# Optimization experiments

Measured on AMD Instinct MI355X. Metric: run time of the kernel, lower is better.

The kernel has to match this reference:

```python
import jax, jax.numpy as jnp
import numpy as np

EPS = 1e-7  # tf.keras.backend.epsilon()
DEGREE = 5
SCALE_BASE = 1.0
SCALE_LEGENDRE = 1.0


def legendre_basis(x, degree):
    # min/max normalization over the feature axis -> x_norm in [-1, 1]
    x_min = jnp.min(x, axis=-1, keepdims=True)
    x_max = jnp.max(x, axis=-1, keepdims=True)
    x_norm = 2.0 * (x - x_min) / (x_max - x_min + EPS) - 1.0
    polys = [jnp.ones_like(x_norm), x_norm]
    for n in range(2, degree + 1):
        p_n = ((2 * n - 1) * x_norm * polys[-1] - (n - 1) * polys[-2]) / n
        polys.append(p_n)
    return jnp.stack(polys, axis=-1)  # [b, i, degree+1]


def setup_inputs() -> dict:
    key = jax.random.key(0)
    k1, k2, k3 = jax.random.split(key, 3)
    b, i, o, d = 4096, 1024, 1024, DEGREE + 1
    x = jax.random.normal(k1, (b, i), dtype=jnp.float32)
    # HeUniform: limit = sqrt(6 / fan_in)
    lim_b = np.sqrt(6.0 / i)
    base_weight = jax.random.uniform(k2, (i, o), dtype=jnp.float32, minval=-lim_b, maxval=lim_b)
    legendre_weight = jax.random.uniform(k3, (i, o, d), dtype=jnp.float32, minval=-lim_b, maxval=lim_b)
    return {"x": x, "base_weight": base_weight, "legendre_weight": legendre_weight}


def reference(x, base_weight, legendre_weight):
    base_output = jax.nn.silu(x @ base_weight)  # [b, o]
    basis = legendre_basis(x, DEGREE)  # [b, i, d]
    # 'bi,iod,bid->bo' == fold x into the basis then contract (i, d)
    xb = x[..., None] * basis  # [b, i, d]
    legendre_output = jnp.einsum('bid,iod->bo', xb, legendre_weight)
    return SCALE_BASE * base_output + SCALE_LEGENDRE * legendre_output
```

## Files before the change

### kernel.cpp

```cpp
#include <hip/hip_runtime.h>
#include <stdint.h>

typedef unsigned short u16;
typedef unsigned int   u32;
typedef __attribute__((ext_vector_type(8))) short bhalf8;
typedef __attribute__((ext_vector_type(4))) float f32x4;

#define B_ROWS 4096
#define I_DIM  1024
#define O_DIM  1024
#define N_D    6
#define K_LEG  (I_DIM * N_D)

#define BM 256
#define BN 256
#define BK 32
#define NU 56
#define SLOT_BYTES 32768
#define LDS_BYTES  131072

__device__ __forceinline__ u16 f2b(float f) {
  u32 u = __float_as_uint(f);
  return (u16)((u + 0x7fffu + ((u >> 16) & 1u)) >> 16);
}

__device__ __forceinline__ void gld_lds16(const void* g, void* l) {
  __builtin_amdgcn_global_load_lds(
      (const __attribute__((address_space(1))) u32*)(uintptr_t)g,
      (__attribute__((address_space(3))) u32*)(u32)(uintptr_t)l, 16, 0, 0);
}

__global__ void k_prep_bbT(const float* __restrict__ bw, u16* __restrict__ Bb) {
  __shared__ float t[32][33];
  const int bx = blockIdx.x & 31, by = blockIdx.x >> 5;
  const int i0 = by * 32, o0 = bx * 32;
  const int c = threadIdx.x & 31, r0 = threadIdx.x >> 5;
  #pragma unroll
  for (int k = 0; k < 4; ++k) {
    int r = r0 + k * 8;
    t[r][c] = bw[(size_t)(i0 + r) * O_DIM + o0 + c];
  }
  __syncthreads();
  #pragma unroll
  for (int k = 0; k < 4; ++k) {
    int r = r0 + k * 8;
    Bb[(size_t)(o0 + r) * I_DIM + i0 + c] = f2b(t[c][r]);
  }
}

#define RS 201
__global__ void k_prep_blT(const float* __restrict__ lw, u16* __restrict__ Bl) {
  __shared__ float t[32 * RS];
  const int bx = blockIdx.x & 31, by = blockIdx.x >> 5;
  const int i0 = by * 32, o0 = bx * 32;
  for (int q = threadIdx.x; q < 32 * 48; q += 256) {
    int ri = q / 48, s4 = q % 48;
    float4 v = *(const float4*)(lw + (size_t)(i0 + ri) * (O_DIM * N_D) + o0 * N_D + s4 * 4);
    float* p = t + ri * RS + s4 * 4;
    p[0] = v.x; p[1] = v.y; p[2] = v.z; p[3] = v.w;
  }
  __syncthreads();
  for (int q = threadIdx.x; q < 32 * 96; q += 256) {
    int ro = q / 96, k = q % 96;
    int e0 = 2 * k, e1 = 2 * k + 1;
    float v0 = t[(e0 / 6) * RS + ro * 6 + (e0 % 6)];
    float v1 = t[(e1 / 6) * RS + ro * 6 + (e1 % 6)];
    u32* dst = (u32*)(Bl + (size_t)(o0 + ro) * K_LEG + i0 * N_D);
    dst[k] = (u32)f2b(v0) | ((u32)f2b(v1) << 16);
  }
}

__global__ void k_prep_basis(const float* __restrict__ x,
                             u16* __restrict__ Ab, u16* __restrict__ Al) {
  int b = blockIdx.x;
  int t = threadIdx.x;
  float4 v = ((const float4*)(x + (size_t)b * I_DIM))[t];
  float mn = fminf(fminf(v.x, v.y), fminf(v.z, v.w));
  float mx = fmaxf(fmaxf(v.x, v.y), fmaxf(v.z, v.w));
  #pragma unroll
  for (int off = 32; off > 0; off >>= 1) {
    mn = fminf(mn, __shfl_xor(mn, off, 64));
    mx = fmaxf(mx, __shfl_xor(mx, off, 64));
  }
  __shared__ float smn[4], smx[4];
  if ((t & 63) == 0) { smn[t >> 6] = mn; smx[t >> 6] = mx; }
  __syncthreads();
  mn = fminf(fminf(smn[0], smn[1]), fminf(smn[2], smn[3]));
  mx = fmaxf(fmaxf(smx[0], smx[1]), fmaxf(smx[2], smx[3]));
  float sc = 2.0f / (mx - mn + 1e-7f);

  float xs[4] = {v.x, v.y, v.z, v.w};
  u32 lb[12];
  #pragma unroll
  for (int e = 0; e < 4; ++e) {
    float xv = xs[e];
    float xn = (xv - mn) * sc - 1.0f;
    float p0 = 1.0f, p1 = xn;
    float p2 = (3.0f * xn * p1 - 1.0f * p0) * (1.0f / 2.0f);
    float p3 = (5.0f * xn * p2 - 2.0f * p1) * (1.0f / 3.0f);
    float p4 = (7.0f * xn * p3 - 3.0f * p2) * (1.0f / 4.0f);
    float p5 = (9.0f * xn * p4 - 4.0f * p3) * (1.0f / 5.0f);
    lb[e * 3 + 0] = (u32)f2b(xv * p0) | ((u32)f2b(xv * p1) << 16);
    lb[e * 3 + 1] = (u32)f2b(xv * p2) | ((u32)f2b(xv * p3) << 16);
    lb[e * 3 + 2] = (u32)f2b(xv * p4) | ((u32)f2b(xv * p5) << 16);
  }
  u32 a0 = (u32)f2b(xs[0]) | ((u32)f2b(xs[1]) << 16);
  u32 a1 = (u32)f2b(xs[2]) | ((u32)f2b(xs[3]) << 16);
  *(uint2*)(Ab + (size_t)b * I_DIM + t * 4) = make_uint2(a0, a1);
  uint4* dl = (uint4*)(Al + (size_t)b * K_LEG + t * 24);
  dl[0] = make_uint4(lb[0], lb[1], lb[2], lb[3]);
  dl[1] = make_uint4(lb[4], lb[5], lb[6], lb[7]);
  dl[2] = make_uint4(lb[8], lb[9], lb[10], lb[11]);
}

__global__ __launch_bounds__(512, 2) void k_gemm(
    const u16* __restrict__ Ab, const u16* __restrict__ Bb,
    const u16* __restrict__ Al, const u16* __restrict__ Bl,
    float* __restrict__ out, float* __restrict__ P) {
  extern __shared__ char lds[];

  const int tid  = threadIdx.x;
  const int wave = tid >> 6;
  const int lane = tid & 63;
  const int wm = wave >> 2;
  const int wn = wave & 3;
  const int rr = lane & 15;
  const int kg = lane >> 4;

  const int bid   = blockIdx.x;
  const int bx    = bid >> 4;
  const int by    = (bid >> 2) & 3;
  const int split = bid & 3;
  const size_t brow = (size_t)bx * BM;
  const size_t bcol = (size_t)by * BN;
  const bool s0 = (split == 0);
  const int legbase = s0 ? 0 : (24 + 56 * (split - 1));

  const int r4 = tid >> 2;
  const size_t cs = (size_t)((((tid & 3) ^ ((r4 >> 1) & 3))) * 8);
  const size_t ar0 = brow + r4,        ar1 = brow + 128 + r4;
  const size_t bc0 = bcol + r4,        bc1 = bcol + 128 + r4;
  char* const l0 = lds + (u32)wave * 1024;

  auto stage = [&](int v) {
    const u16 *sa, *sb; size_t ldk, koff;
    if (s0 && v < 32) { sa = Ab; sb = Bb; ldk = I_DIM; koff = (size_t)v * BK; }
    else {
      size_t lv = s0 ? (size_t)(v - 32) : (size_t)(legbase + v);
      sa = Al; sb = Bl; ldk = K_LEG; koff = lv * BK;
    }
    char* d = l0 + (size_t)(v & 3) * SLOT_BYTES;
    gld_lds16(sa + ar0 * ldk + koff + cs, d);
    gld_lds16(sa + ar1 * ldk + koff + cs, d + 8192);
    gld_lds16(sb + bc0 * ldk + koff + cs, d + 16384);
    gld_lds16(sb + bc1 * ldk + koff + cs, d + 24576);
  };

  const u32 axor  = (u32)((kg ^ ((rr >> 1) & 3)) * 16);
  const u32 abase = (u32)((wm * 128 + rr) * 64) + axor;
  const u32 bbase = 16384u + (u32)((wn * 64 + rr) * 64) + axor;

  f32x4 acc[8][4] = {};

  stage(0); stage(1); stage(2);

#define KITER(u, DO_STAGE, VM)  do {                                          \
    if (DO_STAGE) stage((u) + 3);                                             \
    asm volatile("s_waitcnt vmcnt(" #VM ")" ::: "memory");                    \
    __builtin_amdgcn_s_barrier();                                             \
    asm volatile("" ::: "memory");                                            \
    const char* p_ = lds + (size_t)((u) & 3) * SLOT_BYTES;                    \
    bhalf8 af_[8], bf_[4];                                                    \
    _Pragma("unroll")                                                         \
    for (int n = 0; n < 4; ++n) bf_[n] = *(const bhalf8*)(p_ + bbase + n * 1024); \
    _Pragma("unroll")                                                         \
    for (int m = 0; m < 8; ++m) af_[m] = *(const bhalf8*)(p_ + abase + m * 1024); \
    __builtin_amdgcn_s_setprio(1);                                            \
    _Pragma("unroll")                                                         \
    for (int m = 0; m < 8; ++m)                                               \
      _Pragma("unroll")                                                       \
      for (int n = 0; n < 4; ++n)                                             \
        acc[m][n] = __builtin_amdgcn_mfma_f32_16x16x32_bf16(af_[m], bf_[n], acc[m][n], 0, 0, 0); \
    __builtin_amdgcn_s_setprio(0);                                            \
    asm volatile("s_waitcnt lgkmcnt(0)" ::: "memory");                        \
    __builtin_amdgcn_s_barrier();                                             \
  } while (0)

  for (int u = 0; u < NU - 3; ++u) {
    if (s0 && u == 32) {
      #pragma unroll
      for (int m = 0; m < 8; ++m)
        #pragma unroll
        for (int n = 0; n < 4; ++n)
          #pragma unroll
          for (int j = 0; j < 4; ++j) {
            float v = acc[m][n][j];
            acc[m][n][j] = v / (1.0f + __expf(-v));
          }
    }
    KITER(u, true, 12);
  }
  KITER(53, false, 8);
  KITER(54, false, 4);
  KITER(55, false, 0);
#undef KITER

  float* dst = s0 ? out : (P + (size_t)(split - 1) * ((size_t)B_ROWS * O_DIM));
  #pragma unroll
  for (int m = 0; m < 8; ++m)
    #pragma unroll
    for (int n = 0; n < 4; ++n) {
      const size_t r0 = brow + wm * 128 + m * 16 + kg * 4;
      const size_t c  = bcol + wn * 64 + n * 16 + rr;
      #pragma unroll
      for (int j = 0; j < 4; ++j)
        dst[(r0 + j) * O_DIM + c] = acc[m][n][j];
    }
}

__global__ void k_reduce(float* __restrict__ out, const float* __restrict__ P) {
  const size_t i = (size_t)blockIdx.x * 256 + threadIdx.x;
  const size_t NE = (size_t)B_ROWS * O_DIM / 4;
  float4 a = ((const float4*)out)[i];
  float4 b = ((const float4*)P)[i];
  float4 c = ((const float4*)P)[i + NE];
  float4 d = ((const float4*)P)[i + 2 * NE];
  a.x += b.x + c.x + d.x;  a.y += b.y + c.y + d.y;
  a.z += b.z + c.z + d.z;  a.w += b.w + c.w + d.w;
  ((float4*)out)[i] = a;
}

extern "C" void kernel_launch(void* const* d_in, const int* in_sizes, int n_in,
                              void* d_out, int out_size, void* d_ws, size_t ws_size,
                              hipStream_t stream) {
  const float* x  = (const float*)d_in[0];
  const float* bw = (const float*)d_in[1];
  const float* lw = (const float*)d_in[2];
  float* out = (float*)d_out;

  char* w = (char*)d_ws;
  u16*  Ab = (u16*)(w);
  u16*  Al = (u16*)(w + (size_t)8   * 1024 * 1024);
  u16*  Bb = (u16*)(w + (size_t)56  * 1024 * 1024);
  u16*  Bl = (u16*)(w + (size_t)58  * 1024 * 1024);
  float* P = (float*)(w + (size_t)72 * 1024 * 1024);

  hipFuncSetAttribute((const void*)k_gemm,
                      hipFuncAttributeMaxDynamicSharedMemorySize, LDS_BYTES);

  k_prep_bbT  <<<dim3(1024), 256, 0, stream>>>(bw, Bb);
  k_prep_blT  <<<dim3(1024), 256, 0, stream>>>(lw, Bl);
  k_prep_basis<<<dim3(B_ROWS), 256, 0, stream>>>(x, Ab, Al);
  k_gemm      <<<dim3(4 * (B_ROWS / BM) * (O_DIM / BN)), 512, LDS_BYTES, stream>>>(Ab, Bb, Al, Bl, out, P);
  k_reduce    <<<dim3((B_ROWS * O_DIM / 4) / 256), 256, 0, stream>>>(out, P);
}
```

Measured before the change: 118.0 us.

## Split GEMM k-iteration into two phases with interleaved staging; merge weight prep kernels

Each k-step of the main GEMM becomes two half-phases over the top and bottom four m-tiles. The global-to-LDS loads for A and B are split across the two phases so that LDS reads, async copies and MFMA work interleave more finely. Global pointers are now advanced incrementally instead of recomputed per stage. The two weight transpose/convert kernels are merged into one launch to save a kernel launch. In exchange there are more barriers per k-step, and the vmcnt accounting changes, which risks both ordering bugs and added sync overhead.

```diff
diff --git a/kernel.cpp b/kernel.cpp
--- a/kernel.cpp
+++ b/kernel.cpp
@@ -30,43 +30,44 @@
       (__attribute__((address_space(3))) u32*)(u32)(uintptr_t)l, 16, 0, 0);
 }
 
-__global__ void k_prep_bbT(const float* __restrict__ bw, u16* __restrict__ Bb) {
-  __shared__ float t[32][33];
-  const int bx = blockIdx.x & 31, by = blockIdx.x >> 5;
-  const int i0 = by * 32, o0 = bx * 32;
-  const int c = threadIdx.x & 31, r0 = threadIdx.x >> 5;
-  #pragma unroll
-  for (int k = 0; k < 4; ++k) {
-    int r = r0 + k * 8;
-    t[r][c] = bw[(size_t)(i0 + r) * O_DIM + o0 + c];
-  }
-  __syncthreads();
-  #pragma unroll
-  for (int k = 0; k < 4; ++k) {
-    int r = r0 + k * 8;
-    Bb[(size_t)(o0 + r) * I_DIM + i0 + c] = f2b(t[c][r]);
-  }
-}
-
 #define RS 201
-__global__ void k_prep_blT(const float* __restrict__ lw, u16* __restrict__ Bl) {
+__global__ void k_prep_w(const float* __restrict__ bw, const float* __restrict__ lw,
+                         u16* __restrict__ Bb, u16* __restrict__ Bl) {
   __shared__ float t[32 * RS];
-  const int bx = blockIdx.x & 31, by = blockIdx.x >> 5;
-  const int i0 = by * 32, o0 = bx * 32;
-  for (int q = threadIdx.x; q < 32 * 48; q += 256) {
-    int ri = q / 48, s4 = q % 48;
-    float4 v = *(const float4*)(lw + (size_t)(i0 + ri) * (O_DIM * N_D) + o0 * N_D + s4 * 4);
-    float* p = t + ri * RS + s4 * 4;
-    p[0] = v.x; p[1] = v.y; p[2] = v.z; p[3] = v.w;
-  }
-  __syncthreads();
-  for (int q = threadIdx.x; q < 32 * 96; q += 256) {
-    int ro = q / 96, k = q % 96;
-    int e0 = 2 * k, e1 = 2 * k + 1;
-    float v0 = t[(e0 / 6) * RS + ro * 6 + (e0 % 6)];
-    float v1 = t[(e1 / 6) * RS + ro * 6 + (e1 % 6)];
-    u32* dst = (u32*)(Bl + (size_t)(o0 + ro) * K_LEG + i0 * N_D);
-    dst[k] = (u32)f2b(v0) | ((u32)f2b(v1) << 16);
+  if (blockIdx.x < 1024) {
+    const int bx = blockIdx.x & 31, by = blockIdx.x >> 5;
+    const int i0 = by * 32, o0 = bx * 32;
+    const int c = threadIdx.x & 31, r0 = threadIdx.x >> 5;
+    #pragma unroll
+    for (int k = 0; k < 4; ++k) {
+      int r = r0 + k * 8;
+      t[r * 33 + c] = bw[(size_t)(i0 + r) * O_DIM + o0 + c];
+    }
+    __syncthreads();
+    #pragma unroll
+    for (int k = 0; k < 4; ++k) {
+      int r = r0 + k * 8;
+      Bb[(size_t)(o0 + r) * I_DIM + i0 + c] = f2b(t[c * 33 + r]);
+    }
+  } else {
+    const int blk = blockIdx.x - 1024;
+    const int bx = blk & 31, by = blk >> 5;
+    const int i0 = by * 32, o0 = bx * 32;
+    for (int q = threadIdx.x; q < 32 * 48; q += 256) {
+      int ri = q / 48, s4 = q % 48;
+      float4 v = *(const float4*)(lw + (size_t)(i0 + ri) * (O_DIM * N_D) + o0 * N_D + s4 * 4);
+      float* p = t + ri * RS + s4 * 4;
+      p[0] = v.x; p[1] = v.y; p[2] = v.z; p[3] = v.w;
+    }
+    __syncthreads();
+    for (int q = threadIdx.x; q < 32 * 96; q += 256) {
+      int ro = q / 96, k = q % 96;
+      int e0 = 2 * k, e1 = 2 * k + 1;
+      float v0 = t[(e0 / 6) * RS + ro * 6 + (e0 % 6)];
+      float v1 = t[(e1 / 6) * RS + ro * 6 + (e1 % 6)];
+      u32* dst = (u32*)(Bl + (size_t)(o0 + ro) * K_LEG + i0 * N_D);
+      dst[k] = (u32)f2b(v0) | ((u32)f2b(v1) << 16);
+    }
   }
 }
 
@@ -138,51 +139,79 @@
 
   const int r4 = tid >> 2;
   const size_t cs = (size_t)((((tid & 3) ^ ((r4 >> 1) & 3))) * 8);
-  const size_t ar0 = brow + r4,        ar1 = brow + 128 + r4;
-  const size_t bc0 = bcol + r4,        bc1 = bcol + 128 + r4;
   char* const l0 = lds + (u32)wave * 1024;
 
-  auto stage = [&](int v) {
-    const u16 *sa, *sb; size_t ldk, koff;
-    if (s0 && v < 32) { sa = Ab; sb = Bb; ldk = I_DIM; koff = (size_t)v * BK; }
-    else {
-      size_t lv = s0 ? (size_t)(v - 32) : (size_t)(legbase + v);
-      sa = Al; sb = Bl; ldk = K_LEG; koff = lv * BK;
-    }
-    char* d = l0 + (size_t)(v & 3) * SLOT_BYTES;
-    gld_lds16(sa + ar0 * ldk + koff + cs, d);
-    gld_lds16(sa + ar1 * ldk + koff + cs, d + 8192);
-    gld_lds16(sb + bc0 * ldk + koff + cs, d + 16384);
-    gld_lds16(sb + bc1 * ldk + koff + cs, d + 24576);
+  const u16 *gA0, *gA1, *gB0, *gB1;
+  auto set_ptrs = [&](const u16* A, const u16* Bt, size_t ldk, size_t kt) {
+    const size_t ko = kt * BK + cs;
+    gA0 = A  + (brow + r4) * ldk + ko;
+    gA1 = A  + (brow + 128 + r4) * ldk + ko;
+    gB0 = Bt + (bcol + r4) * ldk + ko;
+    gB1 = Bt + (bcol + 128 + r4) * ldk + ko;
   };
+  if (s0) set_ptrs(Ab, Bb, I_DIM, 0);
+  else    set_ptrs(Al, Bl, K_LEG, (size_t)legbase);
 
   const u32 axor  = (u32)((kg ^ ((rr >> 1) & 3)) * 16);
   const u32 abase = (u32)((wm * 128 + rr) * 64) + axor;
   const u32 bbase = 16384u + (u32)((wn * 64 + rr) * 64) + axor;
 
   f32x4 acc[8][4] = {};
-
-  stage(0); stage(1); stage(2);
-
-#define KITER(u, DO_STAGE, VM)  do {                                          \
-    if (DO_STAGE) stage((u) + 3);                                             \
-    asm volatile("s_waitcnt vmcnt(" #VM ")" ::: "memory");                    \
-    __builtin_amdgcn_s_barrier();                                             \
+  bhalf8 af_[4], af2_[4], bf_[4];
+
+  #pragma unroll
+  for (int v = 0; v < 3; ++v) {
+    char* d = l0 + (size_t)v * SLOT_BYTES;
+    gld_lds16(gA0, d);          gld_lds16(gA1, d + 8192);
+    gld_lds16(gB0, d + 16384);  gld_lds16(gB1, d + 24576);
+    gA0 += BK; gA1 += BK; gB0 += BK; gB1 += BK;
+  }
+  asm volatile("s_waitcnt vmcnt(8)" ::: "memory");
+  __builtin_amdgcn_s_barrier();
+
+#define PH0(u, DO_STAGE) do {                                                 \
+    const char* p_ = lds + (size_t)((u) & 3) * SLOT_BYTES;                    \
+    _Pragma("unroll")                                                         \
+    for (int n = 0; n < 4; ++n) bf_[n] = *(const bhalf8*)(p_ + bbase + n * 1024); \
+    _Pragma("unroll")                                                         \
+    for (int m = 0; m < 4; ++m) af_[m] = *(const bhalf8*)(p_ + abase + m * 1024); \
+    if (DO_STAGE) {                                                           \
+      char* d_ = l0 + (size_t)(((u) + 3) & 3) * SLOT_BYTES;                   \
+      gld_lds16(gA0, d_); gld_lds16(gA1, d_ + 8192);                          \
+    }                                                                         \
     asm volatile("" ::: "memory");                                            \
-    const char* p_ = lds + (size_t)((u) & 3) * SLOT_BYTES;                    \
-    bhalf8 af_[8], bf_[4];                                                    \
-    _Pragma("unroll")                                                         \
-    for (int n = 0; n < 4; ++n) bf_[n] = *(const bhalf8*)(p_ + bbase + n * 1024); \
-    _Pragma("unroll")                                                         \
-    for (int m = 0; m < 8; ++m) af_[m] = *(const bhalf8*)(p_ + abase + m * 1024); \
+    __builtin_amdgcn_s_barrier();                                             \
+    asm volatile("s_waitcnt lgkmcnt(0)" ::: "memory");                        \
     __builtin_amdgcn_s_setprio(1);                                            \
     _Pragma("unroll")                                                         \
-    for (int m = 0; m < 8; ++m)                                               \
+    for (int m = 0; m < 4; ++m)                                               \
       _Pragma("unroll")                                                       \
       for (int n = 0; n < 4; ++n)                                             \
         acc[m][n] = __builtin_amdgcn_mfma_f32_16x16x32_bf16(af_[m], bf_[n], acc[m][n], 0, 0, 0); \
     __builtin_amdgcn_s_setprio(0);                                            \
+    __builtin_amdgcn_s_barrier();                                             \
+  } while (0)
+
+#define PH1(u, DO_STAGE, VM) do {                                             \
+    const char* p_ = lds + (size_t)((u) & 3) * SLOT_BYTES;                    \
+    _Pragma("unroll")                                                         \
+    for (int m = 0; m < 4; ++m) af2_[m] = *(const bhalf8*)(p_ + abase + (4 + m) * 1024); \
+    if (DO_STAGE) {                                                           \
+      char* d_ = l0 + (size_t)(((u) + 3) & 3) * SLOT_BYTES;                   \
+      gld_lds16(gB0, d_ + 16384); gld_lds16(gB1, d_ + 24576);                 \
+      if (s0 && (u) + 4 == 32) set_ptrs(Al, Bl, K_LEG, 0);                    \
+      else { gA0 += BK; gA1 += BK; gB0 += BK; gB1 += BK; }                    \
+    }                                                                         \
+    asm volatile("s_waitcnt vmcnt(" #VM ")" ::: "memory");                    \
+    __builtin_amdgcn_s_barrier();                                             \
     asm volatile("s_waitcnt lgkmcnt(0)" ::: "memory");                        \
+    __builtin_amdgcn_s_setprio(1);                                            \
+    _Pragma("unroll")                                                         \
+    for (int m = 0; m < 4; ++m)                                               \
+      _Pragma("unroll")                                                       \
+      for (int n = 0; n < 4; ++n)                                             \
+        acc[4 + m][n] = __builtin_amdgcn_mfma_f32_16x16x32_bf16(af2_[m], bf_[n], acc[4 + m][n], 0, 0, 0); \
+    __builtin_amdgcn_s_setprio(0);                                            \
     __builtin_amdgcn_s_barrier();                                             \
   } while (0)
 
@@ -198,12 +227,14 @@
             acc[m][n][j] = v / (1.0f + __expf(-v));
           }
     }
-    KITER(u, true, 12);
-  }
-  KITER(53, false, 8);
-  KITER(54, false, 4);
-  KITER(55, false, 0);
-#undef KITER
+    PH0(u, true);
+    PH1(u, true, 8);
+  }
+  PH0(53, false); PH1(53, false, 4);
+  PH0(54, false); PH1(54, false, 0);
+  PH0(55, false); PH1(55, false, 0);
+#undef PH0
+#undef PH1
 
   float* dst = s0 ? out : (P + (size_t)(split - 1) * ((size_t)B_ROWS * O_DIM));
   #pragma unroll
@@ -248,8 +279,7 @@
   hipFuncSetAttribute((const void*)k_gemm,
                       hipFuncAttributeMaxDynamicSharedMemorySize, LDS_BYTES);
 
-  k_prep_bbT  <<<dim3(1024), 256, 0, stream>>>(bw, Bb);
-  k_prep_blT  <<<dim3(1024), 256, 0, stream>>>(lw, Bl);
+  k_prep_w    <<<dim3(2048), 256, 0, stream>>>(bw, lw, Bb, Bl);
   k_prep_basis<<<dim3(B_ROWS), 256, 0, stream>>>(x, Ab, Al);
   k_gemm      <<<dim3(4 * (B_ROWS / BM) * (O_DIM / BN)), 512, LDS_BYTES, stream>>>(Ab, Bb, Al, Bl, out, P);
   k_reduce    <<<dim3((B_ROWS * O_DIM / 4) / 256), 256, 0, stream>>>(out, P);
```

New measurement: 112.8 us. 4.5% less time.
